# Optimization experiments

Hardware: AMD Instinct MI355X
Metric: run time of the kernel (lower is better)

## Reference

```python
import jax, jax.numpy as jnp
import numpy as np

NUM_HEADS = 8


def _attn(q, k, v, scale):
    # q: [B,H,Nq,d], k/v: [B,H,Nk,d]
    a = jax.nn.softmax(jnp.einsum('bhqd,bhkd->bhqk', q, k) * scale, axis=-1)
    return jnp.einsum('bhqk,bhkd->bhqd', a, v)


def setup_inputs() -> dict:
    key = jax.random.key(0)
    k1, k2, k3 = jax.random.split(key, 3)
    B, N, C = 8, 1024, 768
    x = jax.random.normal(k1, (B, N, C), dtype=jnp.float32)
    w_qkv = jax.random.normal(k2, (3 * C, C), dtype=jnp.float32) * 0.02
    w_proj = jax.random.normal(k3, (C, C), dtype=jnp.float32) * 0.02
    b_proj = jnp.zeros((C,), dtype=jnp.float32)
    return {"x": x, "w_qkv": w_qkv, "w_proj": w_proj, "b_proj": b_proj}


def reference(x, w_qkv, w_proj, b_proj):
    B, N, C = x.shape
    H = NUM_HEADS
    hd = C // H            # full head dim (scale uses this, per the source)
    g = hd // 3            # per-group head dim
    scale = hd ** (-0.5)

    qkv = (x @ w_qkv.T).reshape(B, N, 3, H, hd).transpose(2, 0, 3, 1, 4)  # [3,B,H,N,hd]
    q, k, v = qkv[0], qkv[1], qkv[2]

    q3, q4, q5 = q[..., :g], q[..., g:2 * g], q[..., 2 * g:]
    k3, k4, k5 = k[..., :g], k[..., g:2 * g], k[..., 2 * g:]
    v3, v4, v5 = v[..., :g], v[..., g:2 * g], v[..., 2 * g:]

    def merge(o):  # [B,H,N,g] -> [B,N,H*g]
        return o.transpose(0, 2, 1, 3).reshape(B, N, C // 3)

    x3 = merge(_attn(q4, jnp.concatenate([k3, k4], axis=2), jnp.concatenate([v3, v4], axis=2), scale))
    x4 = merge(_attn(q5, jnp.concatenate([k3, k5], axis=2), jnp.concatenate([v3, v5], axis=2), scale))
    x5 = merge(_attn(q5, jnp.concatenate([k4, k5], axis=2), jnp.concatenate([v4, v5], axis=2), scale))

    out = jnp.concatenate([x3, x4, x5], axis=2)
    return out @ w_proj.T + b_proj
```

## Files before the change

kernel.cpp:

```cpp
#include <hip/hip_runtime.h>
#include <hip/hip_bf16.h>

typedef unsigned short u16;
typedef __attribute__((ext_vector_type(8))) short short8;
typedef __attribute__((ext_vector_type(4))) float f32x4;

__device__ __forceinline__ u16 f2b(float f) {
  union { float f; unsigned u; } a; a.f = f;
  unsigned r = a.u + 0x7fffu + ((a.u >> 16) & 1u);
  return (u16)(r >> 16);
}

__device__ __forceinline__ unsigned pkbf16(float lo, float hi) {
  unsigned r;
  asm("v_cvt_pk_bf16_f32 %0, %1, %2" : "=v"(r) : "v"(lo), "v"(hi));
  return r;
}

#define GLD_LDS16(gp, lp) __builtin_amdgcn_global_load_lds( \
    (const __attribute__((address_space(1))) void*)(gp),    \
    (__attribute__((address_space(3))) void*)(lp), 16, 0, 0)

__global__ __launch_bounds__(256) void cvt3(
    const float* __restrict__ x, const float* __restrict__ wq, const float* __restrict__ wp,
    u16* __restrict__ xb, u16* __restrict__ wqb, u16* __restrict__ wpb)
{
  const int NX = 8192 * 768 / 4, NQ = 2304 * 768 / 4, NP = 768 * 768 / 4;
  int i = blockIdx.x * 256 + threadIdx.x;
  const float* src; u16* dst; int j;
  if (i < NX)            { src = x;  dst = xb;  j = i; }
  else if (i < NX + NQ)  { src = wq; dst = wqb; j = i - NX; }
  else if (i < NX + NQ + NP) { src = wp; dst = wpb; j = i - NX - NQ; }
  else return;
  float4 v = *(const float4*)&src[(size_t)j * 4];
  u16 o[4] = { f2b(v.x), f2b(v.y), f2b(v.z), f2b(v.w) };
  *(uint2*)&dst[(size_t)j * 4] = *(uint2*)o;
}

__global__ __launch_bounds__(256) void gemm_bt(
    const u16* __restrict__ A, const u16* __restrict__ Bt,
    u16* __restrict__ Cb, float* __restrict__ Cf, const float* __restrict__ bias,
    int M, int N, int K)
{
  __shared__ u16 Al[128 * 32];
  __shared__ u16 Bl[128 * 32];
  const int tid = threadIdx.x;
  const int lane = tid & 63, wave = tid >> 6;
  const int wr = wave >> 1, wc = wave & 1;
  const int g = lane >> 4, c16 = lane & 15;
  const int m0 = blockIdx.y * 128, n0 = blockIdx.x * 128;

  f32x4 acc[4][4] = {};

  const int c0 = tid, c1 = tid + 256;
  const int r0 = c0 >> 2, o0 = (c0 & 3) * 8;
  const int r1 = c1 >> 2, o1 = (c1 & 3) * 8;
  const u16* a0 = A + (size_t)(m0 + r0) * K + o0;
  const u16* a1 = A + (size_t)(m0 + r1) * K + o1;
  const u16* b0 = Bt + (size_t)(n0 + r0) * K + o0;
  const u16* b1 = Bt + (size_t)(n0 + r1) * K + o1;

  for (int k0 = 0; k0 < K; k0 += 32) {
    GLD_LDS16(a0 + k0, Al + c0 * 8);
    GLD_LDS16(a1 + k0, Al + c1 * 8);
    GLD_LDS16(b0 + k0, Bl + c0 * 8);
    GLD_LDS16(b1 + k0, Bl + c1 * 8);
    __syncthreads();
    short8 af[4], bfr[4];
#pragma unroll
    for (int m = 0; m < 4; ++m)
      af[m] = *(const short8*)&Al[(wr * 64 + m * 16 + c16) * 32 + g * 8];
#pragma unroll
    for (int n = 0; n < 4; ++n)
      bfr[n] = *(const short8*)&Bl[(wc * 64 + n * 16 + c16) * 32 + g * 8];
#pragma unroll
    for (int m = 0; m < 4; ++m)
#pragma unroll
      for (int n = 0; n < 4; ++n)
        acc[m][n] = __builtin_amdgcn_mfma_f32_16x16x32_bf16(af[m], bfr[n], acc[m][n], 0, 0, 0);
    __syncthreads();
  }

  if (Cb) {
#pragma unroll
    for (int m = 0; m < 4; ++m) {
      const int row = m0 + wr * 64 + m * 16 + g * 4;
#pragma unroll
      for (int n = 0; n < 4; ++n) {
        const int col = n0 + wc * 64 + n * 16 + c16;
#pragma unroll
        for (int j = 0; j < 4; ++j)
          Cb[(size_t)(row + j) * N + col] = f2b(acc[m][n][j]);
      }
    }
  } else {
#pragma unroll
    for (int m = 0; m < 4; ++m) {
      const int row = m0 + wr * 64 + m * 16 + g * 4;
#pragma unroll
      for (int n = 0; n < 4; ++n) {
        const int col = n0 + wc * 64 + n * 16 + c16;
        const float bb = bias[col];
#pragma unroll
        for (int j = 0; j < 4; ++j)
          Cf[(size_t)(row + j) * N + col] = acc[m][n][j] + bb;
      }
    }
  }
}

__global__ __launch_bounds__(256) void vtrans(const u16* __restrict__ qkv, u16* __restrict__ vt)
{
  __shared__ u16 Vtl[96 * 72];
  const int tid = threadIdx.x;
  const int bh = blockIdx.x >> 4, nt = blockIdx.x & 15;
  const int b = bh >> 3, h = bh & 7;
  const int n0 = nt * 64;
  const size_t tb = (size_t)b * 1024;
#pragma unroll
  for (int i = 0; i < 3; ++i) {
    int c = tid + i * 256;
    int key = c / 12, cc = c % 12;
    uint4 v = *(const uint4*)&qkv[(tb + n0 + key) * 2304 + 1536 + h * 96 + cc * 8];
    union { uint4 u; u16 s[8]; } cv; cv.u = v;
#pragma unroll
    for (int j = 0; j < 8; ++j)
      Vtl[(cc * 8 + j) * 72 + key] = cv.s[j];
  }
  __syncthreads();
#pragma unroll
  for (int i = 0; i < 3; ++i) {
    int c = tid + i * 256;
    int d = c >> 3, c2 = c & 7;
    int chunk = c2 >> 2;
    int kA = ((c2 & 1) << 4) | ((c2 & 2) << 1);
    const u16* src = &Vtl[d * 72 + c2 * 8];
    size_t base = ((size_t)bh * 96 + d) * 1024 + n0 + chunk * 32;
    *(uint2*)&vt[base + kA]     = *(const uint2*)(src);
    *(uint2*)&vt[base + kA + 8] = *(const uint2*)(src + 4);
  }
}

__global__ __launch_bounds__(256, 2) void attn_kernel(
    const u16* __restrict__ qkv, const u16* __restrict__ vt, u16* __restrict__ feat)
{
  __shared__ u16 Kl[3][64 * 40];
  __shared__ u16 Vl[96 * 72];

  const int tid = threadIdx.x;
  const int lane = tid & 63;
  const int g = lane >> 4, c16 = lane & 15;
  const int qt = blockIdx.x, bh = blockIdx.y;
  const int b = bh >> 3, h = bh & 7;
  const int q0 = qt * 128 + (tid >> 6) * 32;
  const size_t tb = (size_t)b * 1024;

  short8 qf[2][2];
#pragma unroll
  for (int qs = 0; qs < 2; ++qs)
#pragma unroll
    for (int m = 0; m < 2; ++m)
      qf[qs][m] = *(const short8*)&qkv[(tb + q0 + m * 16 + c16) * 2304 + h * 96 + 32 + 32 * qs + 8 * g];

  f32x4 acc[4][2][2] = {};
  float lsum[4][2] = {};

  int kk_key[3], kk_cc[3], vv_d[3], vv_c[3];
#pragma unroll
  for (int i = 0; i < 3; ++i) {
    int c = tid + i * 256;
    kk_key[i] = c / 12; kk_cc[i] = c % 12;
    vv_d[i] = c >> 3;   vv_c[i] = c & 7;
  }
  uint4 kst[3], vst[3];
#pragma unroll
  for (int i = 0; i < 3; ++i) {
    kst[i] = *(const uint4*)&qkv[(tb + kk_key[i]) * 2304 + 768 + h * 96 + kk_cc[i] * 8];
    vst[i] = *(const uint4*)&vt[((size_t)bh * 96 + vv_d[i]) * 1024 + vv_c[i] * 8];
  }

  const float c2s = 0.14724447f;
  const int ATT[5] = {0, 0, 1, 3, 2};
  const int QS[5]  = {0, 0, 1, 1, 1};
  const int KS[5]  = {0, 1, 0, 2, 1};

  for (int t = 0; t < 16; ++t) {
    __syncthreads();
#pragma unroll
    for (int i = 0; i < 3; ++i) {
      int part = kk_cc[i] >> 2, g4 = kk_cc[i] & 3;
      *(uint4*)&Kl[part][kk_key[i] * 40 + g4 * 8] = kst[i];
      *(uint4*)&Vl[vv_d[i] * 72 + vv_c[i] * 8] = vst[i];
    }
    if (t < 15) {
      int kv0 = (t + 1) * 64;
#pragma unroll
      for (int i = 0; i < 3; ++i) {
        kst[i] = *(const uint4*)&qkv[(tb + kv0 + kk_key[i]) * 2304 + 768 + h * 96 + kk_cc[i] * 8];
        vst[i] = *(const uint4*)&vt[((size_t)bh * 96 + vv_d[i]) * 1024 + kv0 + vv_c[i] * 8];
      }
    }
    __syncthreads();

#pragma unroll
    for (int u = 0; u < 5; ++u) {
      const int att = ATT[u], qs = QS[u], ks = KS[u];
      short8 kf[4], vf[2][2];
#pragma unroll
      for (int n = 0; n < 4; ++n)
        kf[n] = *(const short8*)&Kl[ks][(n * 16 + c16) * 40 + g * 8];
#pragma unroll
      for (int n = 0; n < 2; ++n)
#pragma unroll
        for (int kk = 0; kk < 2; ++kk)
          vf[n][kk] = *(const short8*)&Vl[(ks * 32 + n * 16 + c16) * 72 + kk * 32 + g * 8];

      const f32x4 z = {0.f, 0.f, 0.f, 0.f};
#pragma unroll
      for (int m = 0; m < 2; ++m) {
        f32x4 St[4];
#pragma unroll
        for (int n = 0; n < 4; ++n)
          St[n] = __builtin_amdgcn_mfma_f32_16x16x32_bf16(kf[n], qf[qs][m], z, 0, 0, 0);
        float p[4][4];
#pragma unroll
        for (int n = 0; n < 4; ++n)
#pragma unroll
          for (int r = 0; r < 4; ++r) {
            p[n][r] = __builtin_amdgcn_exp2f(St[n][r] * c2s);
            lsum[att][m] += p[n][r];
          }
        short8 pa[2];
#pragma unroll
        for (int kk = 0; kk < 2; ++kk) {
          union { unsigned u[4]; short8 s; } w;
          w.u[0] = pkbf16(p[2 * kk][0],     p[2 * kk][1]);
          w.u[1] = pkbf16(p[2 * kk][2],     p[2 * kk][3]);
          w.u[2] = pkbf16(p[2 * kk + 1][0], p[2 * kk + 1][1]);
          w.u[3] = pkbf16(p[2 * kk + 1][2], p[2 * kk + 1][3]);
          pa[kk] = w.s;
        }
#pragma unroll
        for (int n = 0; n < 2; ++n)
#pragma unroll
          for (int kk = 0; kk < 2; ++kk)
            acc[att][m][n] = __builtin_amdgcn_mfma_f32_16x16x32_bf16(pa[kk], vf[n][kk], acc[att][m][n], 0, 0, 0);
      }
    }
  }

#pragma unroll
  for (int m = 0; m < 2; ++m) {
    lsum[1][m] += lsum[3][m];
    lsum[2][m] += lsum[3][m];
#pragma unroll
    for (int n = 0; n < 2; ++n) {
      acc[1][m][n] += acc[3][m][n];
      acc[2][m][n] += acc[3][m][n];
    }
  }

  const int srcb = (lane & 48) | ((lane >> 2) & 12);
  float inv[3][2][4];
#pragma unroll
  for (int a = 0; a < 3; ++a)
#pragma unroll
    for (int m = 0; m < 2; ++m) {
      float v = lsum[a][m];
      v += __shfl_xor(v, 16);
      v += __shfl_xor(v, 32);
#pragma unroll
      for (int r = 0; r < 4; ++r)
        inv[a][m][r] = 1.0f / __shfl(v, srcb | r);
    }

#pragma unroll
  for (int a = 0; a < 3; ++a)
#pragma unroll
    for (int m = 0; m < 2; ++m)
#pragma unroll
      for (int n = 0; n < 2; ++n)
#pragma unroll
        for (int r = 0; r < 4; ++r) {
          int row = q0 + m * 16 + g * 4 + r;
          int col = a * 256 + h * 32 + n * 16 + c16;
          feat[(tb + row) * 768 + col] = f2b(acc[a][m][n][r] * inv[a][m][r]);
        }
}

extern "C" void kernel_launch(void* const* d_in, const int* in_sizes, int n_in,
                              void* d_out, int out_size, void* d_ws, size_t ws_size,
                              hipStream_t stream) {
  const float* x  = (const float*)d_in[0];
  const float* wq = (const float*)d_in[1];
  const float* wp = (const float*)d_in[2];
  const float* bp = (const float*)d_in[3];
  float* out = (float*)d_out;

  char* ws = (char*)d_ws;
  u16* xb    = (u16*)(ws);
  u16* wqb   = (u16*)(ws + 12582912);
  u16* wpb   = (u16*)(ws + 16121856);
  u16* qkvb  = (u16*)(ws + 17301504);
  u16* vtb   = (u16*)(ws + 55050240);
  u16* featb = xb;

  cvt3<<<8448, 256, 0, stream>>>(x, wq, wp, xb, wqb, wpb);
  gemm_bt<<<dim3(18, 64), 256, 0, stream>>>(xb, wqb, qkvb, nullptr, nullptr, 8192, 2304, 768);
  vtrans<<<1024, 256, 0, stream>>>(qkvb, vtb);
  attn_kernel<<<dim3(8, 64), 256, 0, stream>>>(qkvb, vtb, featb);
  gemm_bt<<<dim3(6, 64), 256, 0, stream>>>(featb, wpb, nullptr, out, bp, 8192, 768, 768);
}
```

Before: 191.8 us.

## Fold softmax scale into Q weights, use MFMA row sums, smaller query tiles

Pre-multiplies the Q rows of the QKV weight by the softmax scale during bf16 conversion, so the attention kernel no longer multiplies each score before exp2. Row sums of probabilities are now computed with an extra MFMA against a ones vector, which removes the scalar accumulation and the cross-lane shuffle reduction. Each wave now handles 16 query rows instead of 32, giving 1024 blocks with a 3-blocks-per-CU launch bound, and s_setprio is raised around the MFMA sections. In exchange, K/V tiles are loaded from global memory twice as often per query row, and the row sums are taken from the bf16-rounded probabilities rather than the fp32 values.

```diff
diff --git a/kernel.cpp b/kernel.cpp
--- a/kernel.cpp
+++ b/kernel.cpp
@@ -28,12 +28,14 @@
   const int NX = 8192 * 768 / 4, NQ = 2304 * 768 / 4, NP = 768 * 768 / 4;
   int i = blockIdx.x * 256 + threadIdx.x;
   const float* src; u16* dst; int j;
+  float sc = 1.0f;
   if (i < NX)            { src = x;  dst = xb;  j = i; }
-  else if (i < NX + NQ)  { src = wq; dst = wqb; j = i - NX; }
+  else if (i < NX + NQ)  { src = wq; dst = wqb; j = i - NX;
+                           if (j < 147456) sc = 0.14724447f; }
   else if (i < NX + NQ + NP) { src = wp; dst = wpb; j = i - NX - NQ; }
   else return;
   float4 v = *(const float4*)&src[(size_t)j * 4];
-  u16 o[4] = { f2b(v.x), f2b(v.y), f2b(v.z), f2b(v.w) };
+  u16 o[4] = { f2b(v.x * sc), f2b(v.y * sc), f2b(v.z * sc), f2b(v.w * sc) };
   *(uint2*)&dst[(size_t)j * 4] = *(uint2*)o;
 }
 
@@ -141,7 +143,7 @@
   }
 }
 
-__global__ __launch_bounds__(256, 2) void attn_kernel(
+__global__ __launch_bounds__(256, 3) void attn_kernel(
     const u16* __restrict__ qkv, const u16* __restrict__ vt, u16* __restrict__ feat)
 {
   __shared__ u16 Kl[3][64 * 40];
@@ -150,20 +152,23 @@
   const int tid = threadIdx.x;
   const int lane = tid & 63;
   const int g = lane >> 4, c16 = lane & 15;
-  const int qt = blockIdx.x, bh = blockIdx.y;
-  const int b = bh >> 3, h = bh & 7;
-  const int q0 = qt * 128 + (tid >> 6) * 32;
+  const int id = blockIdx.x;
+  const int h = id & 7, qt = (id >> 3) & 15, b = id >> 7;
+  const int bh = b * 8 + h;
+  const int q0 = qt * 64 + (tid >> 6) * 16;
   const size_t tb = (size_t)b * 1024;
 
-  short8 qf[2][2];
+  short8 qf[2];
 #pragma unroll
   for (int qs = 0; qs < 2; ++qs)
-#pragma unroll
-    for (int m = 0; m < 2; ++m)
-      qf[qs][m] = *(const short8*)&qkv[(tb + q0 + m * 16 + c16) * 2304 + h * 96 + 32 + 32 * qs + 8 * g];
-
-  f32x4 acc[4][2][2] = {};
-  float lsum[4][2] = {};
+    qf[qs] = *(const short8*)&qkv[(tb + q0 + c16) * 2304 + h * 96 + 32 + 32 * qs + 8 * g];
+
+  short8 ones;
+#pragma unroll
+  for (int i = 0; i < 8; ++i) ones[i] = (short)0x3F80;
+
+  f32x4 acc[4][2] = {};
+  f32x4 lsv[4] = {};
 
   int kk_key[3], kk_cc[3], vv_d[3], vv_c[3];
 #pragma unroll
@@ -179,7 +184,6 @@
     vst[i] = *(const uint4*)&vt[((size_t)bh * 96 + vv_d[i]) * 1024 + vv_c[i] * 8];
   }
 
-  const float c2s = 0.14724447f;
   const int ATT[5] = {0, 0, 1, 3, 2};
   const int QS[5]  = {0, 0, 1, 1, 1};
   const int KS[5]  = {0, 1, 0, 2, 1};
@@ -216,76 +220,57 @@
           vf[n][kk] = *(const short8*)&Vl[(ks * 32 + n * 16 + c16) * 72 + kk * 32 + g * 8];
 
       const f32x4 z = {0.f, 0.f, 0.f, 0.f};
-#pragma unroll
-      for (int m = 0; m < 2; ++m) {
-        f32x4 St[4];
-#pragma unroll
-        for (int n = 0; n < 4; ++n)
-          St[n] = __builtin_amdgcn_mfma_f32_16x16x32_bf16(kf[n], qf[qs][m], z, 0, 0, 0);
-        float p[4][4];
-#pragma unroll
-        for (int n = 0; n < 4; ++n)
-#pragma unroll
-          for (int r = 0; r < 4; ++r) {
-            p[n][r] = __builtin_amdgcn_exp2f(St[n][r] * c2s);
-            lsum[att][m] += p[n][r];
-          }
-        short8 pa[2];
-#pragma unroll
-        for (int kk = 0; kk < 2; ++kk) {
-          union { unsigned u[4]; short8 s; } w;
-          w.u[0] = pkbf16(p[2 * kk][0],     p[2 * kk][1]);
-          w.u[1] = pkbf16(p[2 * kk][2],     p[2 * kk][3]);
-          w.u[2] = pkbf16(p[2 * kk + 1][0], p[2 * kk + 1][1]);
-          w.u[3] = pkbf16(p[2 * kk + 1][2], p[2 * kk + 1][3]);
-          pa[kk] = w.s;
-        }
-#pragma unroll
-        for (int n = 0; n < 2; ++n)
-#pragma unroll
-          for (int kk = 0; kk < 2; ++kk)
-            acc[att][m][n] = __builtin_amdgcn_mfma_f32_16x16x32_bf16(pa[kk], vf[n][kk], acc[att][m][n], 0, 0, 0);
-      }
-    }
-  }
-
-#pragma unroll
-  for (int m = 0; m < 2; ++m) {
-    lsum[1][m] += lsum[3][m];
-    lsum[2][m] += lsum[3][m];
-#pragma unroll
-    for (int n = 0; n < 2; ++n) {
-      acc[1][m][n] += acc[3][m][n];
-      acc[2][m][n] += acc[3][m][n];
-    }
-  }
-
-  const int srcb = (lane & 48) | ((lane >> 2) & 12);
-  float inv[3][2][4];
-#pragma unroll
-  for (int a = 0; a < 3; ++a)
-#pragma unroll
-    for (int m = 0; m < 2; ++m) {
-      float v = lsum[a][m];
-      v += __shfl_xor(v, 16);
-      v += __shfl_xor(v, 32);
-#pragma unroll
-      for (int r = 0; r < 4; ++r)
-        inv[a][m][r] = 1.0f / __shfl(v, srcb | r);
-    }
-
-#pragma unroll
-  for (int a = 0; a < 3; ++a)
-#pragma unroll
-    for (int m = 0; m < 2; ++m)
+      f32x4 St[4];
+      __builtin_amdgcn_s_setprio(1);
+#pragma unroll
+      for (int n = 0; n < 4; ++n)
+        St[n] = __builtin_amdgcn_mfma_f32_16x16x32_bf16(kf[n], qf[qs], z, 0, 0, 0);
+      __builtin_amdgcn_s_setprio(0);
+      short8 pa[2];
+#pragma unroll
+      for (int kk = 0; kk < 2; ++kk) {
+        union { unsigned u[4]; short8 s; } w;
+        w.u[0] = pkbf16(__builtin_amdgcn_exp2f(St[2 * kk][0]),     __builtin_amdgcn_exp2f(St[2 * kk][1]));
+        w.u[1] = pkbf16(__builtin_amdgcn_exp2f(St[2 * kk][2]),     __builtin_amdgcn_exp2f(St[2 * kk][3]));
+        w.u[2] = pkbf16(__builtin_amdgcn_exp2f(St[2 * kk + 1][0]), __builtin_amdgcn_exp2f(St[2 * kk + 1][1]));
+        w.u[3] = pkbf16(__builtin_amdgcn_exp2f(St[2 * kk + 1][2]), __builtin_amdgcn_exp2f(St[2 * kk + 1][3]));
+        pa[kk] = w.s;
+      }
+      __builtin_amdgcn_s_setprio(1);
 #pragma unroll
       for (int n = 0; n < 2; ++n)
 #pragma unroll
-        for (int r = 0; r < 4; ++r) {
-          int row = q0 + m * 16 + g * 4 + r;
-          int col = a * 256 + h * 32 + n * 16 + c16;
-          feat[(tb + row) * 768 + col] = f2b(acc[a][m][n][r] * inv[a][m][r]);
-        }
+        for (int kk = 0; kk < 2; ++kk)
+          acc[att][n] = __builtin_amdgcn_mfma_f32_16x16x32_bf16(pa[kk], vf[n][kk], acc[att][n], 0, 0, 0);
+#pragma unroll
+      for (int kk = 0; kk < 2; ++kk)
+        lsv[att] = __builtin_amdgcn_mfma_f32_16x16x32_bf16(pa[kk], ones, lsv[att], 0, 0, 0);
+      __builtin_amdgcn_s_setprio(0);
+    }
+  }
+
+  lsv[1] += lsv[3];
+  lsv[2] += lsv[3];
+#pragma unroll
+  for (int n = 0; n < 2; ++n) {
+    acc[1][n] += acc[3][n];
+    acc[2][n] += acc[3][n];
+  }
+
+#pragma unroll
+  for (int a = 0; a < 3; ++a) {
+    f32x4 inv;
+#pragma unroll
+    for (int r = 0; r < 4; ++r) inv[r] = 1.0f / lsv[a][r];
+#pragma unroll
+    for (int n = 0; n < 2; ++n)
+#pragma unroll
+      for (int r = 0; r < 4; ++r) {
+        int row = q0 + g * 4 + r;
+        int col = a * 256 + h * 32 + n * 16 + c16;
+        feat[(tb + row) * 768 + col] = f2b(acc[a][n][r] * inv[r]);
+      }
+  }
 }
 
 extern "C" void kernel_launch(void* const* d_in, const int* in_sizes, int n_in,
@@ -308,6 +293,6 @@
   cvt3<<<8448, 256, 0, stream>>>(x, wq, wp, xb, wqb, wpb);
   gemm_bt<<<dim3(18, 64), 256, 0, stream>>>(xb, wqb, qkvb, nullptr, nullptr, 8192, 2304, 768);
   vtrans<<<1024, 256, 0, stream>>>(qkvb, vtb);
-  attn_kernel<<<dim3(8, 64), 256, 0, stream>>>(qkvb, vtb, featb);
+  attn_kernel<<<1024, 256, 0, stream>>>(qkvb, vtb, featb);
   gemm_bt<<<dim3(6, 64), 256, 0, stream>>>(featb, wpb, nullptr, out, bp, 8192, 768, 768);
 }
```

Result: slower. 206.1 us (+7.5%).
